# Kernel optimization log

Measured on AMD Instinct MI355X. Metric: run time of the kernel, lower is better.

Reference implementation:

```python
import jax, jax.numpy as jnp
import numpy as np

I = J = K = 400   # tensor_shape
R = 16            # CP rank
N_QUERIES = 100000


def setup_inputs() -> dict:
    key = jax.random.key(0)
    k1, k2, k3, k4 = jax.random.split(key, 4)
    # factors: Parameter(torch.randn(rank, n_dim) / 100.0)
    U = jax.random.normal(k1, (R, I), dtype=jnp.float32) / 100.0
    V = jax.random.normal(k2, (R, J), dtype=jnp.float32) / 100.0
    W = jax.random.normal(k3, (R, K), dtype=jnp.float32) / 100.0
    # batched (i, j, k) coordinate triples (train() feeds rows of data[:, :-1])
    index = jax.random.randint(k4, (N_QUERIES, 3), 0, I, dtype=jnp.int64)
    return {"U": U, "V": V, "W": W, "index": index}


def reference(U, V, W, index):
    # Faithful to the original math: sum over ranks of outer products
    # re_tensor[i,j,k] = sum_r U[r,i] * V[r,j] * W[r,k]
    # (the original builds this with a python loop over ranks + repeat();
    #  einsum expresses the identical dense reconstruction)
    dense = jnp.einsum('ri,rj,rk->ijk', U, V, W)  # [I, J, K]
    # gather the requested (i, j, k) entries
    return dense[index[:, 0], index[:, 1], index[:, 2]]  # [N]
```

## Files before the change

kernel.cpp:

```cpp
#include <hip/hip_runtime.h>


#define RANK 16
#define DIM  400
#define PER  (RANK * DIM)

__global__ void cp_transpose_factors(const float* __restrict__ U,
                                     const float* __restrict__ V,
                                     const float* __restrict__ W,
                                     float* __restrict__ ws) {
    int tid = blockIdx.x * blockDim.x + threadIdx.x;
    if (tid >= 3 * PER) return;
    int f   = tid / PER;
    int rem = tid - f * PER;
    int r   = rem / DIM;
    int i   = rem - r * DIM;
    const float* src = (f == 0) ? U : (f == 1) ? V : W;
    ws[f * PER + i * RANK + r] = src[rem];
}

__global__ void cp_gather(const float* __restrict__ ws,
                          const int* __restrict__ idx,
                          float* __restrict__ out, int n) {
    int t = blockIdx.x * blockDim.x + threadIdx.x;
    if (t >= n) return;
    int i = idx[3 * t + 0];
    int j = idx[3 * t + 1];
    int k = idx[3 * t + 2];
    const float4* Ut = (const float4*)(ws);
    const float4* Vt = (const float4*)(ws + PER);
    const float4* Wt = (const float4*)(ws + 2 * PER);
    float acc = 0.0f;
#pragma unroll
    for (int q = 0; q < 4; ++q) {
        float4 u = Ut[i * 4 + q];
        float4 v = Vt[j * 4 + q];
        float4 w = Wt[k * 4 + q];
        acc = fmaf(u.x, v.x * w.x, acc);
        acc = fmaf(u.y, v.y * w.y, acc);
        acc = fmaf(u.z, v.z * w.z, acc);
        acc = fmaf(u.w, v.w * w.w, acc);
    }
    out[t] = acc;
}

__global__ void cp_gather_direct(const float* __restrict__ U,
                                 const float* __restrict__ V,
                                 const float* __restrict__ W,
                                 const int* __restrict__ idx,
                                 float* __restrict__ out, int n) {
    int t = blockIdx.x * blockDim.x + threadIdx.x;
    if (t >= n) return;
    int i = idx[3 * t + 0];
    int j = idx[3 * t + 1];
    int k = idx[3 * t + 2];
    float acc = 0.0f;
#pragma unroll
    for (int r = 0; r < RANK; ++r) {
        acc = fmaf(U[r * DIM + i], V[r * DIM + j] * W[r * DIM + k], acc);
    }
    out[t] = acc;
}

extern "C" void kernel_launch(void* const* d_in, const int* in_sizes, int n_in,
                              void* d_out, int out_size, void* d_ws, size_t ws_size,
                              hipStream_t stream) {
    const float* U   = (const float*)d_in[0];
    const float* V   = (const float*)d_in[1];
    const float* W   = (const float*)d_in[2];
    const int*   idx = (const int*)d_in[3];
    float*       out = (float*)d_out;
    const int n = out_size;

    if (ws_size >= (size_t)(3 * PER) * sizeof(float)) {
        float* ws = (float*)d_ws;
        {
            int total = 3 * PER;
            int blk = 256;
            cp_transpose_factors<<<(total + blk - 1) / blk, blk, 0, stream>>>(U, V, W, ws);
        }
        {
            int blk = 256;
            cp_gather<<<(n + blk - 1) / blk, blk, 0, stream>>>(ws, idx, out, n);
        }
    } else {
        int blk = 256;
        cp_gather_direct<<<(n + blk - 1) / blk, blk, 0, stream>>>(U, V, W, idx, out, n);
    }
}
```

Baseline: 63.84 us.

## Fuse transpose and gather into one kernel staging factors in LDS

Replaces the two-kernel path (transpose factors into workspace, then gather with float4 loads) with a single kernel. Each 512-thread block copies all three factor matrices (75 KB) into shared memory, then each thread evaluates one query from LDS. This removes a kernel launch and the dependent workspace round trip. In exchange, every block reloads 75 KB of factors, and the large LDS footprint limits resident blocks per CU.

```diff
diff --git a/kernel.cpp b/kernel.cpp
--- a/kernel.cpp
+++ b/kernel.cpp
@@ -4,60 +4,46 @@
 #define RANK 16
 #define DIM  400
 #define PER  (RANK * DIM)
+#define PER4 (PER / 4)
+#define BLOCK 512
+#define QPB   512
 
-__global__ void cp_transpose_factors(const float* __restrict__ U,
-                                     const float* __restrict__ V,
-                                     const float* __restrict__ W,
-                                     float* __restrict__ ws) {
-    int tid = blockIdx.x * blockDim.x + threadIdx.x;
-    if (tid >= 3 * PER) return;
-    int f   = tid / PER;
-    int rem = tid - f * PER;
-    int r   = rem / DIM;
-    int i   = rem - r * DIM;
-    const float* src = (f == 0) ? U : (f == 1) ? V : W;
-    ws[f * PER + i * RANK + r] = src[rem];
-}
+__global__ __launch_bounds__(BLOCK)
+void cp_fused(const float* __restrict__ U,
+              const float* __restrict__ V,
+              const float* __restrict__ W,
+              const int* __restrict__ idx,
+              float* __restrict__ out, int n) {
+    __shared__ float lds[3 * PER];
 
-__global__ void cp_gather(const float* __restrict__ ws,
-                          const int* __restrict__ idx,
-                          float* __restrict__ out, int n) {
-    int t = blockIdx.x * blockDim.x + threadIdx.x;
+    {
+        const float4* U4 = (const float4*)U;
+        const float4* V4 = (const float4*)V;
+        const float4* W4 = (const float4*)W;
+        float4* L4 = (float4*)lds;
+        for (int c = threadIdx.x; c < PER4; c += BLOCK) {
+            L4[c]            = U4[c];
+            L4[c + PER4]     = V4[c];
+            L4[c + 2 * PER4] = W4[c];
+        }
+    }
+    __syncthreads();
+
+    int t = blockIdx.x * QPB + threadIdx.x;
     if (t >= n) return;
+
     int i = idx[3 * t + 0];
     int j = idx[3 * t + 1];
     int k = idx[3 * t + 2];
-    const float4* Ut = (const float4*)(ws);
-    const float4* Vt = (const float4*)(ws + PER);
-    const float4* Wt = (const float4*)(ws + 2 * PER);
-    float acc = 0.0f;
-#pragma unroll
-    for (int q = 0; q < 4; ++q) {
-        float4 u = Ut[i * 4 + q];
-        float4 v = Vt[j * 4 + q];
-        float4 w = Wt[k * 4 + q];
-        acc = fmaf(u.x, v.x * w.x, acc);
-        acc = fmaf(u.y, v.y * w.y, acc);
-        acc = fmaf(u.z, v.z * w.z, acc);
-        acc = fmaf(u.w, v.w * w.w, acc);
-    }
-    out[t] = acc;
-}
 
-__global__ void cp_gather_direct(const float* __restrict__ U,
-                                 const float* __restrict__ V,
-                                 const float* __restrict__ W,
-                                 const int* __restrict__ idx,
-                                 float* __restrict__ out, int n) {
-    int t = blockIdx.x * blockDim.x + threadIdx.x;
-    if (t >= n) return;
-    int i = idx[3 * t + 0];
-    int j = idx[3 * t + 1];
-    int k = idx[3 * t + 2];
+    const float* Ul = lds;
+    const float* Vl = lds + PER;
+    const float* Wl = lds + 2 * PER;
+
     float acc = 0.0f;
 #pragma unroll
     for (int r = 0; r < RANK; ++r) {
-        acc = fmaf(U[r * DIM + i], V[r * DIM + j] * W[r * DIM + k], acc);
+        acc = fmaf(Ul[r * DIM + i], Vl[r * DIM + j] * Wl[r * DIM + k], acc);
     }
     out[t] = acc;
 }
@@ -72,19 +58,6 @@
     float*       out = (float*)d_out;
     const int n = out_size;
 
-    if (ws_size >= (size_t)(3 * PER) * sizeof(float)) {
-        float* ws = (float*)d_ws;
-        {
-            int total = 3 * PER;
-            int blk = 256;
-            cp_transpose_factors<<<(total + blk - 1) / blk, blk, 0, stream>>>(U, V, W, ws);
-        }
-        {
-            int blk = 256;
-            cp_gather<<<(n + blk - 1) / blk, blk, 0, stream>>>(ws, idx, out, n);
-        }
-    } else {
-        int blk = 256;
-        cp_gather_direct<<<(n + blk - 1) / blk, blk, 0, stream>>>(U, V, W, idx, out, n);
-    }
+    int grid = (n + QPB - 1) / QPB;
+    cp_fused<<<grid, BLOCK, 0, stream>>>(U, V, W, idx, out, n);
 }
```

Measured after the change: 61.20 us (median of 2 runs). 1.04x faster.
